# Performance work log

Measured on AMD Instinct MI355X. Metric: run time of the kernel, lower is better.

The kernel has to match this reference:

```python
import jax, jax.numpy as jnp
import numpy as np

N_BR, D, SD, RH, MH, UD, NOBS, B = 4, 256, 64, 64, 128, 16, 25, 32768
LN_EPS = 1e-5

def setup_inputs() -> dict:
    key = jax.random.key(0)
    ks = jax.random.split(key, 16)
    meas_in = D + SD
    rnn_in = RH + UD
    return {
        "z_dyn": jax.random.normal(ks[0], (B, D), jnp.float32),
        "z_static": jax.random.normal(ks[1], (B, SD), jnp.float32),
        "dt": jnp.ones((1,), jnp.float32),
        "ut": jax.random.normal(ks[2], (B, UD), jnp.float32),
        "gates": jax.random.normal(ks[3], (N_BR, D), jnp.float32) * 0.1,
        "W1": jax.random.normal(ks[4], (N_BR, MH, meas_in), jnp.float32) * (1.0 / np.sqrt(meas_in)),
        "b1": jnp.zeros((N_BR, MH), jnp.float32),
        "gamma": jnp.ones((N_BR, MH), jnp.float32),
        "beta": jnp.zeros((N_BR, MH), jnp.float32),
        "W2": jax.random.normal(ks[5], (N_BR, RH, MH), jnp.float32) * (1.0 / np.sqrt(MH)),
        "b2": jnp.zeros((N_BR, RH), jnp.float32),
        "lam_real": jnp.zeros((N_BR, RH), jnp.float32),
        "lam_imag": jax.random.normal(ks[6], (N_BR, RH), jnp.float32) * 0.1,
        "Bmat": jax.random.normal(ks[7], (N_BR, RH, rnn_in), jnp.float32) * (1.0 / np.sqrt(rnn_in)),
        "Wout": jax.random.normal(ks[8], (N_BR, D, RH), jnp.float32) * (1.0 / np.sqrt(RH)),
        "C": jax.random.normal(ks[9], (NOBS, D), jnp.float32) * (1.0 / np.sqrt(D)),
        "D": jax.random.normal(ks[10], (NOBS, UD), jnp.float32) * (1.0 / np.sqrt(UD)),
    }

def reference(z_dyn, z_static, dt, ut, gates, W1, b1, gamma, beta, W2, b2,
              lam_real, lam_imag, Bmat, Wout, C, D):
    ut_dt = ut * dt  # [B,u]
    n, Bsz = gates.shape[0], z_dyn.shape[0]
    # spectral gate per branch: [n,B,d]
    zg = z_dyn[None] * jax.nn.sigmoid(gates)[:, None, :]
    zs = jnp.broadcast_to(z_static[None], (n, Bsz, z_static.shape[-1]))
    x = jnp.concatenate([zg, zs], axis=-1)  # [n,B,meas_in]
    # measurement MLP: Linear -> LayerNorm -> GELU -> Linear
    h = jnp.einsum('nbi,nhi->nbh', x, W1) + b1[:, None, :]
    mu = h.mean(-1, keepdims=True)
    var = ((h - mu) ** 2).mean(-1, keepdims=True)
    h = (h - mu) / jnp.sqrt(var + LN_EPS) * gamma[:, None, :] + beta[:, None, :]
    h = jax.nn.gelu(h, approximate=False)
    g = jnp.einsum('nbh,noh->nbo', h, W2) + b2[:, None, :]  # [n,B,rnn_h]
    u_b = jnp.broadcast_to(ut_dt[None], (n, Bsz, ut_dt.shape[-1]))
    inp = jnp.concatenate([g, u_b], axis=-1)  # [n,B,rnn_h+u]
    b_inp = jnp.einsum('nbi,nhi->nbh', inp, Bmat)
    # complex recurrence step from h0 = 0 (as in forward())
    mag = jax.nn.sigmoid(lam_real) * 0.99
    lam_r = mag * jnp.cos(lam_imag)
    lam_i = mag * jnp.sin(lam_imag)
    h0r = jnp.zeros_like(b_inp)
    h0i = jnp.zeros_like(b_inp)
    h_real = h0r * lam_r[:, None, :] - h0i * lam_i[:, None, :] + b_inp
    # output projection per branch, summed over branches
    z_next = jnp.einsum('nbh,ndh->bd', h_real, Wout)
    yt = z_next @ C.T + ut_dt @ D.T
    return (z_next, yt)
```

## Files before the change

### kernel.cpp

```cpp
#include <hip/hip_runtime.h>
#include <hip/hip_bf16.h>

#define B_ROWS 32768
#define LN_EPS 1e-5f

typedef __bf16 bf16;
using bf16x8 = __attribute__((ext_vector_type(8))) __bf16;
using f32x4  = __attribute__((ext_vector_type(4))) float;


__device__ __forceinline__ float gelu_exact(float x) {
  float s = x * 0.70710678118f;
  float a = fabsf(s);
  float t = __builtin_amdgcn_rcpf(fmaf(0.3275911f, a, 1.0f));
  float p = fmaf(fmaf(fmaf(fmaf(1.061405429f, t, -1.453152027f),
                           t, 1.421413741f), t, -0.284496736f), t, 0.254829592f) * t;
  float e = __expf(-s * s);
  float er = fmaf(-p, e, 1.0f);
  er = copysignf(er, s);
  return 0.5f * x * (1.0f + er);
}

__device__ __forceinline__ float dot64(const float* __restrict__ a,
                                       const float* __restrict__ b) {
  const f32x4* A = (const f32x4*)a;
  const f32x4* B = (const f32x4*)b;
  f32x4 acc = {0.f, 0.f, 0.f, 0.f};
  #pragma unroll
  for (int i = 0; i < 16; ++i) acc += A[i] * B[i];
  return acc[0] + acc[1] + acc[2] + acc[3];
}

__global__ __launch_bounds__(256) void prep_weights1(
    const float* __restrict__ gates, const float* __restrict__ W1,
    const float* __restrict__ Bmat,  const float* __restrict__ W2,
    const float* __restrict__ b2,    const float* __restrict__ Wout,
    const float* __restrict__ Cm,
    bf16* __restrict__ W1sw, float* __restrict__ MtmpT, float* __restrict__ cvec,
    float* __restrict__ CW,  float* __restrict__ BuT)
{
  const int stride = gridDim.x * blockDim.x;
  const int id = blockIdx.x * blockDim.x + threadIdx.x;

  for (int i = id; i < (512 * 320) / 8; i += stride) {
    int m = i & 15, q2 = (i >> 4) & 3, rest = i >> 6;
    int kk = rest % 10, G = rest / 10;
    int n = G * 16 + m, kb = kk * 32 + q2 * 8;
    float4 v0 = *(const float4*)&W1[n * 320 + kb];
    float4 v1 = *(const float4*)&W1[n * 320 + kb + 4];
    float vv[8] = {v0.x, v0.y, v0.z, v0.w, v1.x, v1.y, v1.z, v1.w};
    if (kb < 256) {
      float4 g0 = *(const float4*)&gates[(n >> 7) * 256 + kb];
      float4 g1 = *(const float4*)&gates[(n >> 7) * 256 + kb + 4];
      float gg[8] = {g0.x, g0.y, g0.z, g0.w, g1.x, g1.y, g1.z, g1.w};
      #pragma unroll
      for (int e = 0; e < 8; ++e) vv[e] *= 1.f / (1.f + __expf(-gg[e]));
    }
    bf16x8 o;
    #pragma unroll
    for (int e = 0; e < 8; ++e) o[e] = (bf16)vv[e];
    *(bf16x8*)&W1sw[i * 8] = o;
  }

  for (int i = id; i < 4 * 64 * 128; i += stride) {
    int n = i >> 13, r = (i >> 7) & 63, h = i & 127;
    float s = 0.f;
    for (int j = 0; j < 64; ++j)
      s += Bmat[(n * 64 + r) * 80 + j] * W2[(n * 64 + j) * 128 + h];
    MtmpT[(n * 128 + h) * 64 + r] = s;
  }

  for (int i = id; i < 256; i += stride) {
    int n = i >> 6, r = i & 63;
    cvec[i] = dot64(&Bmat[(n * 64 + r) * 80], &b2[n * 64]);
  }

  for (int i = id; i < 4 * 16 * 64; i += stride) {
    int n = i >> 10, u = (i >> 6) & 15, r = i & 63;
    BuT[i] = Bmat[(n * 64 + r) * 80 + 64 + u];
  }

  for (int i = id; i < 25 * 256; i += stride) {
    int o = i >> 8, nr = i & 255;
    float s = 0.f;
    for (int d = 0; d < 256; ++d)
      s += Cm[o * 256 + d] * Wout[((nr >> 6) * 256 + d) * 64 + (nr & 63)];
    CW[i] = s;
  }
}

__global__ __launch_bounds__(256) void prep_weights2(
    const float* __restrict__ Wout, const float* __restrict__ MtmpT,
    const float* __restrict__ cvec, const float* __restrict__ CW,
    const float* __restrict__ Dm,   const float* __restrict__ BuT,
    bf16* __restrict__ Psw)
{
  const int stride = gridDim.x * blockDim.x;
  const int id = blockIdx.x * blockDim.x + threadIdx.x;
  for (int o = id; o < 320 * 544; o += stride) {
    int e = o & 7, m = (o >> 3) & 15, q2 = (o >> 7) & 3, rest = o >> 9;
    int kk2 = rest % 17, G2 = rest / 17;
    int dd = G2 * 16 + m, cc = kk2 * 32 + q2 * 8 + e;
    float s = 0.f;
    if (dd < 281) {
      const bool isC = (dd >= 256);
      const int oo = dd - 256;
      if (cc < 512) {
        int n = cc >> 7, h = cc & 127;
        const float* a = isC ? &CW[(oo * 4 + n) * 64] : &Wout[(n * 256 + dd) * 64];
        s = dot64(a, &MtmpT[(n * 128 + h) * 64]);
      } else if (cc < 528) {
        int u = cc - 512;
        #pragma unroll
        for (int n = 0; n < 4; ++n) {
          const float* a = isC ? &CW[(oo * 4 + n) * 64] : &Wout[(n * 256 + dd) * 64];
          s += dot64(a, &BuT[(n * 16 + u) * 64]);
        }
        if (isC) s += Dm[oo * 16 + u];
      } else if (cc == 528) {
        #pragma unroll
        for (int n = 0; n < 4; ++n) {
          const float* a = isC ? &CW[(oo * 4 + n) * 64] : &Wout[(n * 256 + dd) * 64];
          s += dot64(a, &cvec[n * 64]);
        }
      }
    }
    Psw[o] = (bf16)s;
  }
}

__global__ __launch_bounds__(256, 2) void fused_main(
    const float* __restrict__ zdyn, const float* __restrict__ zst,
    const float* __restrict__ ut,   const float* __restrict__ dtp,
    const bf16* __restrict__ W1sw,  const bf16* __restrict__ Psw,
    const float* __restrict__ b1,   const float* __restrict__ gamma,
    const float* __restrict__ beta,
    float* __restrict__ Z, float* __restrict__ yt)
{
  __shared__ __align__(16) bf16 Xs[64 * 320];
  __shared__ __align__(16) bf16 Hc[2 * 64 * 128];
  __shared__ __align__(16) bf16 Ht[64 * 32];
  __shared__ __align__(16) float partS[64 * 4];
  __shared__ __align__(16) float partQ[64 * 4];

  const int t = threadIdx.x;
  const int lane = t & 63, m16 = lane & 15, q = lane >> 4;
  const int w = t >> 6;
  const int rowBase = blockIdx.x * 64;

  #pragma unroll
  for (int a = 0; a < 10; ++a) {
    int g = a * 256 + t;
    int row = g / 40, pos = g - row * 40;
    int kk = pos >> 2, pq = pos & 3;
    int lq = pq ^ ((row >> 1) & 3);
    int col = kk * 32 + lq * 8;
    const float* src = (col < 256) ? &zdyn[(size_t)(rowBase + row) * 256 + col]
                                   : &zst[(size_t)(rowBase + row) * 64 + (col - 256)];
    float4 v0 = *(const float4*)src;
    float4 v1 = *(const float4*)(src + 4);
    bf16x8 o;
    o[0]=(bf16)v0.x; o[1]=(bf16)v0.y; o[2]=(bf16)v0.z; o[3]=(bf16)v0.w;
    o[4]=(bf16)v1.x; o[5]=(bf16)v1.y; o[6]=(bf16)v1.z; o[7]=(bf16)v1.w;
    *(bf16x8*)&Xs[(size_t)((kk * 64 + row) * 4 + pq) * 8] = o;
  }
  {
    const float dtv = dtp[0];
    int r = t >> 2, pq = t & 3;
    int lq = pq ^ ((r >> 1) & 3);
    bf16x8 o;
    #pragma unroll
    for (int e = 0; e < 8; ++e) {
      int ci = lq * 8 + e;
      float v = (ci < 16) ? ut[(size_t)(rowBase + r) * 16 + ci] * dtv
                          : (ci == 16 ? 1.f : 0.f);
      o[e] = (bf16)v;
    }
    *(bf16x8*)&Ht[t * 8] = o;
  }
  __syncthreads();

  f32x4 accZ[4][5];
  #pragma unroll
  for (int i = 0; i < 4; ++i)
    #pragma unroll
    for (int j = 0; j < 5; ++j)
      #pragma unroll
      for (int r = 0; r < 4; ++r) accZ[i][j][r] = 0.f;

  f32x4 acc1[4][2];

  auto ph1_step = [&](int c, int kk) {
    bf16x8 bfr[2];
    #pragma unroll
    for (int j = 0; j < 2; ++j) {
      int G = c * 8 + w * 2 + j;
      bfr[j] = *(const bf16x8*)&W1sw[(size_t)(((G * 10 + kk) * 4 + q) * 16 + m16) * 8];
    }
    bf16x8 af[4];
    #pragma unroll
    for (int i = 0; i < 4; ++i) {
      int row = i * 16 + m16;
      af[i] = *(const bf16x8*)&Xs[(size_t)((kk * 64 + row) * 4 + (q ^ ((row >> 1) & 3))) * 8];
    }
    __builtin_amdgcn_s_setprio(1);
    #pragma unroll
    for (int i = 0; i < 4; ++i)
      #pragma unroll
      for (int j = 0; j < 2; ++j)
        acc1[i][j] = __builtin_amdgcn_mfma_f32_16x16x32_bf16(af[i], bfr[j], acc1[i][j], 0, 0, 0);
    __builtin_amdgcn_s_setprio(0);
  };

  auto ph2_step = [&](int cprev, int tk) {
    const int hb = (cprev & 1) * 8192;
    int kk2 = cprev * 4 + tk;
    bf16x8 af[4], bfr[5];
    #pragma unroll
    for (int i = 0; i < 4; ++i) {
      int row = i * 16 + m16;
      af[i] = *(const bf16x8*)&Hc[hb + ((tk * 64 + row) * 4 + (q ^ ((row >> 1) & 3))) * 8];
    }
    #pragma unroll
    for (int j = 0; j < 5; ++j) {
      int G2 = w * 5 + j;
      bfr[j] = *(const bf16x8*)&Psw[(size_t)(((G2 * 17 + kk2) * 4 + q) * 16 + m16) * 8];
    }
    __builtin_amdgcn_s_setprio(1);
    #pragma unroll
    for (int i = 0; i < 4; ++i)
      #pragma unroll
      for (int j = 0; j < 5; ++j)
        accZ[i][j] = __builtin_amdgcn_mfma_f32_16x16x32_bf16(af[i], bfr[j], accZ[i][j], 0, 0, 0);
    __builtin_amdgcn_s_setprio(0);
  };

  auto ln_block = [&](int c) {
    const int hbuf = (c & 1) * 8192;
    float bbj[2], gmj[2], btj[2];
    #pragma unroll
    for (int j = 0; j < 2; ++j) {
      int col = c * 128 + w * 32 + j * 16 + m16;
      bbj[j] = b1[col]; gmj[j] = gamma[col]; btj[j] = beta[col];
    }
    #pragma unroll
    for (int i = 0; i < 4; ++i)
      #pragma unroll
      for (int j = 0; j < 2; ++j)
        #pragma unroll
        for (int rr = 0; rr < 4; ++rr) acc1[i][j][rr] += bbj[j];

    #pragma unroll
    for (int i = 0; i < 4; ++i)
      #pragma unroll
      for (int rr = 0; rr < 4; ++rr) {
        float a0 = acc1[i][0][rr], a1 = acc1[i][1][rr];
        float s  = a0 + a1;
        float s2 = fmaf(a0, a0, a1 * a1);
        #pragma unroll
        for (int m = 1; m <= 8; m <<= 1) {
          s  += __shfl_xor(s,  m);
          s2 += __shfl_xor(s2, m);
        }
        if (m16 == 0) {
          int row = i * 16 + q * 4 + rr;
          partS[row * 4 + w] = s;
          partQ[row * 4 + w] = s2;
        }
      }
    __syncthreads();

    #pragma unroll
    for (int i = 0; i < 4; ++i) {
      #pragma unroll
      for (int rr = 0; rr < 4; ++rr) {
        int row = i * 16 + q * 4 + rr;
        f32x4 ps  = *(const f32x4*)&partS[row * 4];
        f32x4 pq2 = *(const f32x4*)&partQ[row * 4];
        float mu = (ps[0] + ps[1] + ps[2] + ps[3]) * 0.0078125f;
        float qq = (pq2[0] + pq2[1] + pq2[2] + pq2[3]) * 0.0078125f;
        float rs = rsqrtf(fmaxf(qq - mu * mu, 0.f) + LN_EPS);
        int rsw = (row >> 1) & 3;
        #pragma unroll
        for (int j = 0; j < 2; ++j) {
          float v = (acc1[i][j][rr] - mu) * rs;
          v = fmaf(v, gmj[j], btj[j]);
          int lq2 = (j * 2 + (m16 >> 3)) ^ rsw;
          Hc[hbuf + ((w * 64 + row) * 4 + lq2) * 8 + (m16 & 7)] = (bf16)gelu_exact(v);
        }
      }
    }
    __syncthreads();
  };

  #pragma unroll
  for (int i = 0; i < 4; ++i)
    #pragma unroll
    for (int j = 0; j < 2; ++j)
      #pragma unroll
      for (int r = 0; r < 4; ++r) acc1[i][j][r] = 0.f;
  #pragma unroll
  for (int kk = 0; kk < 10; ++kk) ph1_step(0, kk);
  ln_block(0);

  #pragma unroll 1
  for (int c = 1; c < 4; ++c) {
    #pragma unroll
    for (int i = 0; i < 4; ++i)
      #pragma unroll
      for (int j = 0; j < 2; ++j)
        #pragma unroll
        for (int r = 0; r < 4; ++r) acc1[i][j][r] = 0.f;
    #pragma unroll
    for (int s = 0; s < 10; ++s) {
      ph1_step(c, s);
      if (s % 3 == 0) ph2_step(c - 1, s / 3);
    }
    ln_block(c);
  }

  #pragma unroll
  for (int tk = 0; tk < 4; ++tk) ph2_step(3, tk);

  {
    bf16x8 af[4], bfr[5];
    #pragma unroll
    for (int i = 0; i < 4; ++i) {
      int row = i * 16 + m16;
      af[i] = *(const bf16x8*)&Ht[(row * 4 + (q ^ ((row >> 1) & 3))) * 8];
    }
    #pragma unroll
    for (int j = 0; j < 5; ++j) {
      int G2 = w * 5 + j;
      bfr[j] = *(const bf16x8*)&Psw[(size_t)(((G2 * 17 + 16) * 4 + q) * 16 + m16) * 8];
    }
    __builtin_amdgcn_s_setprio(1);
    #pragma unroll
    for (int i = 0; i < 4; ++i)
      #pragma unroll
      for (int j = 0; j < 5; ++j)
        accZ[i][j] = __builtin_amdgcn_mfma_f32_16x16x32_bf16(af[i], bfr[j], accZ[i][j], 0, 0, 0);
    __builtin_amdgcn_s_setprio(0);
  }

  #pragma unroll
  for (int i = 0; i < 4; ++i)
    #pragma unroll
    for (int j = 0; j < 5; ++j) {
      int col = w * 80 + j * 16 + m16;
      #pragma unroll
      for (int rr = 0; rr < 4; ++rr) {
        int row = rowBase + i * 16 + q * 4 + rr;
        if (col < 256) Z[(size_t)row * 256 + col] = accZ[i][j][rr];
        else if (col < 281) yt[(size_t)row * 25 + (col - 256)] = accZ[i][j][rr];
      }
    }
}

extern "C" void kernel_launch(void* const* d_in, const int* in_sizes, int n_in,
                              void* d_out, int out_size, void* d_ws, size_t ws_size,
                              hipStream_t stream) {
  const float* zdyn  = (const float*)d_in[0];
  const float* zst   = (const float*)d_in[1];
  const float* dtp   = (const float*)d_in[2];
  const float* ut    = (const float*)d_in[3];
  const float* gates = (const float*)d_in[4];
  const float* W1    = (const float*)d_in[5];
  const float* b1    = (const float*)d_in[6];
  const float* gamma = (const float*)d_in[7];
  const float* beta  = (const float*)d_in[8];
  const float* W2    = (const float*)d_in[9];
  const float* b2    = (const float*)d_in[10];
  const float* Bmat  = (const float*)d_in[13];
  const float* Wout  = (const float*)d_in[14];
  const float* Cm    = (const float*)d_in[15];
  const float* Dm    = (const float*)d_in[16];

  char* ws = (char*)d_ws;
  bf16*  W1sw  = (bf16*)(ws);
  bf16*  Psw   = (bf16*)(ws + 327680);
  float* MtmpT = (float*)(ws + 675840);
  float* cvec  = (float*)(ws + 806912);
  float* CW    = (float*)(ws + 807936);
  float* BuT   = (float*)(ws + 833536);

  float* Z  = (float*)d_out;
  float* yt = Z + (size_t)B_ROWS * 256;

  hipLaunchKernelGGL(prep_weights1, dim3(128), dim3(256), 0, stream,
                     gates, W1, Bmat, W2, b2, Wout, Cm, W1sw, MtmpT, cvec, CW, BuT);
  hipLaunchKernelGGL(prep_weights2, dim3(256), dim3(256), 0, stream,
                     Wout, MtmpT, cvec, CW, Dm, BuT, Psw);
  hipLaunchKernelGGL(fused_main, dim3(512), dim3(256), 0, stream,
                     zdyn, zst, ut, dtp, W1sw, Psw, b1, gamma, beta, Z, yt);
}
```

Measured before the change: 202.4 us.

## Split each 64-row block across eight waves as a 2x4 wave grid

Doubles the block size of the fused kernel from 256 to 512 threads and splits the 64 rows into two halves per wave-row, so each wave handles 32 rows and a quarter of the columns. Per-wave accumulator registers are halved, which should allow more waves resident per CU and better latency hiding. In exchange, each B-fragment (weights) is loaded by twice as many waves, which adds global/L2 traffic, and barrier cost grows with the larger block.

```diff
diff --git a/kernel.cpp b/kernel.cpp
--- a/kernel.cpp
+++ b/kernel.cpp
@@ -129,7 +129,7 @@
   }
 }
 
-__global__ __launch_bounds__(256, 2) void fused_main(
+__global__ __launch_bounds__(512, 2) void fused_main(
     const float* __restrict__ zdyn, const float* __restrict__ zst,
     const float* __restrict__ ut,   const float* __restrict__ dtp,
     const bf16* __restrict__ W1sw,  const bf16* __restrict__ Psw,
@@ -146,11 +146,13 @@
   const int t = threadIdx.x;
   const int lane = t & 63, m16 = lane & 15, q = lane >> 4;
   const int w = t >> 6;
+  const int wr = w >> 2;
+  const int wc = w & 3;
   const int rowBase = blockIdx.x * 64;
 
   #pragma unroll
-  for (int a = 0; a < 10; ++a) {
-    int g = a * 256 + t;
+  for (int a = 0; a < 5; ++a) {
+    int g = a * 512 + t;
     int row = g / 40, pos = g - row * 40;
     int kk = pos >> 2, pq = pos & 3;
     int lq = pq ^ ((row >> 1) & 3);
@@ -164,7 +166,7 @@
     o[4]=(bf16)v1.x; o[5]=(bf16)v1.y; o[6]=(bf16)v1.z; o[7]=(bf16)v1.w;
     *(bf16x8*)&Xs[(size_t)((kk * 64 + row) * 4 + pq) * 8] = o;
   }
-  {
+  if (t < 256) {
     const float dtv = dtp[0];
     int r = t >> 2, pq = t & 3;
     int lq = pq ^ ((r >> 1) & 3);
@@ -180,32 +182,32 @@
   }
   __syncthreads();
 
-  f32x4 accZ[4][5];
-  #pragma unroll
-  for (int i = 0; i < 4; ++i)
+  f32x4 accZ[2][5];
+  #pragma unroll
+  for (int i = 0; i < 2; ++i)
     #pragma unroll
     for (int j = 0; j < 5; ++j)
       #pragma unroll
       for (int r = 0; r < 4; ++r) accZ[i][j][r] = 0.f;
 
-  f32x4 acc1[4][2];
+  f32x4 acc1[2][2];
 
   auto ph1_step = [&](int c, int kk) {
     bf16x8 bfr[2];
     #pragma unroll
     for (int j = 0; j < 2; ++j) {
-      int G = c * 8 + w * 2 + j;
+      int G = c * 8 + wc * 2 + j;
       bfr[j] = *(const bf16x8*)&W1sw[(size_t)(((G * 10 + kk) * 4 + q) * 16 + m16) * 8];
     }
-    bf16x8 af[4];
-    #pragma unroll
-    for (int i = 0; i < 4; ++i) {
-      int row = i * 16 + m16;
+    bf16x8 af[2];
+    #pragma unroll
+    for (int i = 0; i < 2; ++i) {
+      int row = wr * 32 + i * 16 + m16;
       af[i] = *(const bf16x8*)&Xs[(size_t)((kk * 64 + row) * 4 + (q ^ ((row >> 1) & 3))) * 8];
     }
     __builtin_amdgcn_s_setprio(1);
     #pragma unroll
-    for (int i = 0; i < 4; ++i)
+    for (int i = 0; i < 2; ++i)
       #pragma unroll
       for (int j = 0; j < 2; ++j)
         acc1[i][j] = __builtin_amdgcn_mfma_f32_16x16x32_bf16(af[i], bfr[j], acc1[i][j], 0, 0, 0);
@@ -215,20 +217,20 @@
   auto ph2_step = [&](int cprev, int tk) {
     const int hb = (cprev & 1) * 8192;
     int kk2 = cprev * 4 + tk;
-    bf16x8 af[4], bfr[5];
-    #pragma unroll
-    for (int i = 0; i < 4; ++i) {
-      int row = i * 16 + m16;
+    bf16x8 af[2], bfr[5];
+    #pragma unroll
+    for (int i = 0; i < 2; ++i) {
+      int row = wr * 32 + i * 16 + m16;
       af[i] = *(const bf16x8*)&Hc[hb + ((tk * 64 + row) * 4 + (q ^ ((row >> 1) & 3))) * 8];
     }
     #pragma unroll
     for (int j = 0; j < 5; ++j) {
-      int G2 = w * 5 + j;
+      int G2 = wc * 5 + j;
       bfr[j] = *(const bf16x8*)&Psw[(size_t)(((G2 * 17 + kk2) * 4 + q) * 16 + m16) * 8];
     }
     __builtin_amdgcn_s_setprio(1);
     #pragma unroll
-    for (int i = 0; i < 4; ++i)
+    for (int i = 0; i < 2; ++i)
       #pragma unroll
       for (int j = 0; j < 5; ++j)
         accZ[i][j] = __builtin_amdgcn_mfma_f32_16x16x32_bf16(af[i], bfr[j], accZ[i][j], 0, 0, 0);
@@ -240,18 +242,18 @@
     float bbj[2], gmj[2], btj[2];
     #pragma unroll
     for (int j = 0; j < 2; ++j) {
-      int col = c * 128 + w * 32 + j * 16 + m16;
+      int col = c * 128 + wc * 32 + j * 16 + m16;
       bbj[j] = b1[col]; gmj[j] = gamma[col]; btj[j] = beta[col];
     }
     #pragma unroll
-    for (int i = 0; i < 4; ++i)
+    for (int i = 0; i < 2; ++i)
       #pragma unroll
       for (int j = 0; j < 2; ++j)
         #pragma unroll
         for (int rr = 0; rr < 4; ++rr) acc1[i][j][rr] += bbj[j];
 
     #pragma unroll
-    for (int i = 0; i < 4; ++i)
+    for (int i = 0; i < 2; ++i)
       #pragma unroll
       for (int rr = 0; rr < 4; ++rr) {
         float a0 = acc1[i][0][rr], a1 = acc1[i][1][rr];
@@ -263,18 +265,18 @@
           s2 += __shfl_xor(s2, m);
         }
         if (m16 == 0) {
-          int row = i * 16 + q * 4 + rr;
-          partS[row * 4 + w] = s;
-          partQ[row * 4 + w] = s2;
+          int row = wr * 32 + i * 16 + q * 4 + rr;
+          partS[row * 4 + wc] = s;
+          partQ[row * 4 + wc] = s2;
         }
       }
     __syncthreads();
 
     #pragma unroll
-    for (int i = 0; i < 4; ++i) {
+    for (int i = 0; i < 2; ++i) {
       #pragma unroll
       for (int rr = 0; rr < 4; ++rr) {
-        int row = i * 16 + q * 4 + rr;
+        int row = wr * 32 + i * 16 + q * 4 + rr;
         f32x4 ps  = *(const f32x4*)&partS[row * 4];
         f32x4 pq2 = *(const f32x4*)&partQ[row * 4];
         float mu = (ps[0] + ps[1] + ps[2] + ps[3]) * 0.0078125f;
@@ -286,7 +288,7 @@
           float v = (acc1[i][j][rr] - mu) * rs;
           v = fmaf(v, gmj[j], btj[j]);
           int lq2 = (j * 2 + (m16 >> 3)) ^ rsw;
-          Hc[hbuf + ((w * 64 + row) * 4 + lq2) * 8 + (m16 & 7)] = (bf16)gelu_exact(v);
+          Hc[hbuf + ((wc * 64 + row) * 4 + lq2) * 8 + (m16 & 7)] = (bf16)gelu_exact(v);
         }
       }
     }
@@ -294,7 +296,7 @@
   };
 
   #pragma unroll
-  for (int i = 0; i < 4; ++i)
+  for (int i = 0; i < 2; ++i)
     #pragma unroll
     for (int j = 0; j < 2; ++j)
       #pragma unroll
@@ -306,7 +308,7 @@
   #pragma unroll 1
   for (int c = 1; c < 4; ++c) {
     #pragma unroll
-    for (int i = 0; i < 4; ++i)
+    for (int i = 0; i < 2; ++i)
       #pragma unroll
       for (int j = 0; j < 2; ++j)
         #pragma unroll
@@ -323,20 +325,20 @@
   for (int tk = 0; tk < 4; ++tk) ph2_step(3, tk);
 
   {
-    bf16x8 af[4], bfr[5];
-    #pragma unroll
-    for (int i = 0; i < 4; ++i) {
-      int row = i * 16 + m16;
+    bf16x8 af[2], bfr[5];
+    #pragma unroll
+    for (int i = 0; i < 2; ++i) {
+      int row = wr * 32 + i * 16 + m16;
       af[i] = *(const bf16x8*)&Ht[(row * 4 + (q ^ ((row >> 1) & 3))) * 8];
     }
     #pragma unroll
     for (int j = 0; j < 5; ++j) {
-      int G2 = w * 5 + j;
+      int G2 = wc * 5 + j;
       bfr[j] = *(const bf16x8*)&Psw[(size_t)(((G2 * 17 + 16) * 4 + q) * 16 + m16) * 8];
     }
     __builtin_amdgcn_s_setprio(1);
     #pragma unroll
-    for (int i = 0; i < 4; ++i)
+    for (int i = 0; i < 2; ++i)
       #pragma unroll
       for (int j = 0; j < 5; ++j)
         accZ[i][j] = __builtin_amdgcn_mfma_f32_16x16x32_bf16(af[i], bfr[j], accZ[i][j], 0, 0, 0);
@@ -344,13 +346,13 @@
   }
 
   #pragma unroll
-  for (int i = 0; i < 4; ++i)
+  for (int i = 0; i < 2; ++i)
     #pragma unroll
     for (int j = 0; j < 5; ++j) {
-      int col = w * 80 + j * 16 + m16;
+      int col = wc * 80 + j * 16 + m16;
       #pragma unroll
       for (int rr = 0; rr < 4; ++rr) {
-        int row = rowBase + i * 16 + q * 4 + rr;
+        int row = rowBase + wr * 32 + i * 16 + q * 4 + rr;
         if (col < 256) Z[(size_t)row * 256 + col] = accZ[i][j][rr];
         else if (col < 281) yt[(size_t)row * 25 + (col - 256)] = accZ[i][j][rr];
       }
@@ -391,6 +393,6 @@
                      gates, W1, Bmat, W2, b2, Wout, Cm, W1sw, MtmpT, cvec, CW, BuT);
   hipLaunchKernelGGL(prep_weights2, dim3(256), dim3(256), 0, stream,
                      Wout, MtmpT, cvec, CW, Dm, BuT, Psw);
-  hipLaunchKernelGGL(fused_main, dim3(512), dim3(256), 0, stream,
+  hipLaunchKernelGGL(fused_main, dim3(512), dim3(512), 0, stream,
                      zdyn, zst, ut, dtp, W1sw, Psw, b1, gamma, beta, Z, yt);
 }
```

New measurement: 217.2 us. +7.3%, slower.
